# Kernel optimization log

Hardware: AMD Instinct MI355X
Metric: run time of the kernel (lower is better)

The kernel has to match this reference:

```python
import jax, jax.numpy as jnp
import numpy as np

TS = 6      # texture cube size (hard-coded in module)
S = 256     # image size (NMR default / ref image size)
DIST = 2.732


def _look_at(verts, eye):
    # NMR look_at: camera at eye, looking at origin, up=(0,1,0)
    eye = jnp.asarray(eye, verts.dtype)
    z = -eye / jnp.linalg.norm(eye)
    up = jnp.array([0.0, 1.0, 0.0], verts.dtype)
    x = jnp.cross(up, z)
    x = x / jnp.linalg.norm(x)
    y = jnp.cross(z, x)
    R = jnp.stack([x, y, z])          # rows = camera axes
    return (verts - eye) @ R.T


def _render(verts, faces, tex_flat, eye):
    # verts [V,3], faces [F,3] int, tex_flat [F*TS^3, 3] (tanh already applied)
    v = _look_at(verts, eye)
    fv = v[faces]                      # [F,3,3]
    p0, p1, p2 = fv[:, 0], fv[:, 1], fv[:, 2]
    ps = (2.0 * jnp.arange(S, dtype=verts.dtype) + 1.0 - S) / S
    PX = jnp.broadcast_to(ps[None, :], (S, S)).reshape(-1)      # x right
    PY = jnp.broadcast_to(-ps[:, None], (S, S)).reshape(-1)     # y up (row 0 = top)

    def edge(a, b):
        # signed edge function, [F,HW]
        return ((PX[None, :] - a[:, 0:1]) * (b[:, 1:2] - a[:, 1:2])
                - (PY[None, :] - a[:, 1:2]) * (b[:, 0:1] - a[:, 0:1]))

    e0 = edge(p1, p2)
    e1 = edge(p2, p0)
    e2 = edge(p0, p1)
    # per-face signed area (double area) [F,1]
    area = ((p1[:, 0] - p0[:, 0]) * (p2[:, 1] - p0[:, 1])
            - (p1[:, 1] - p0[:, 1]) * (p2[:, 0] - p0[:, 0]))[:, None]
    ok = jnp.abs(area) > 1e-8
    inv = jnp.where(ok, 1.0 / jnp.where(ok, area, 1.0), 0.0)
    w0, w1, w2 = e0 * inv, e1 * inv, e2 * inv            # barycentric weights
    inside = (w0 >= 0) & (w1 >= 0) & (w2 >= 0) & ok       # both windings (fill_back)
    z = w0 * p0[:, 2:3] + w1 * p1[:, 2:3] + w2 * p2[:, 2:3]
    depth = jnp.where(inside & (z > 0), z, jnp.inf)       # z-buffer candidates
    best = jnp.argmin(depth, axis=0)                      # [HW] winning face
    hit = jnp.take_along_axis(depth, best[None, :], axis=0)[0] < jnp.inf
    wb = jnp.stack([jnp.take_along_axis(w, best[None, :], axis=0)[0]
                    for w in (w0, w1, w2)], axis=-1)       # [HW,3]
    ti = jnp.clip(jnp.round(wb * (TS - 1)), 0, TS - 1).astype(jnp.int32)
    flat = ((best * TS + ti[:, 0]) * TS + ti[:, 1]) * TS + ti[:, 2]
    colors = tex_flat[flat]                                # [HW,3] gather
    img = jnp.where(hit[:, None], colors, 0.0)
    return img.reshape(S, S, 3).transpose(2, 0, 1)[None]   # [1,3,S,S]


def setup_inputs() -> dict:
    key = jax.random.key(0)
    k1, k2, k3, k4, k5 = jax.random.split(key, 5)
    V, F = 252, 500
    return {
        "vertices": jax.random.normal(k1, (1, V, 3), jnp.float32),
        "faces": jax.random.randint(k2, (1, F, 3), 0, V, jnp.int64),
        "textures": jax.random.normal(k3, (1, F, TS, TS, TS, 3), jnp.float32),
        "image_ref": jax.random.uniform(k4, (1, 3, S, S), jnp.float32),
        "image_ref_2": jax.random.uniform(k5, (1, 3, S, S), jnp.float32),
    }


def reference(vertices, faces, textures, image_ref, image_ref_2):
    tex_flat = jnp.tanh(textures[0]).reshape(-1, 3)
    v, f = vertices[0], faces[0]
    # eye = get_points_from_angles(2.732, 180, 0) -> (0, 0, +d)
    img1 = _render(v, f, tex_flat, jnp.array([0.0, 0.0, DIST], jnp.float32))
    loss_one_side = jnp.sum((img1 - image_ref) ** 2)
    # eye = get_points_from_angles(2.732, 0, 0) -> (0, 0, -d)
    img2 = _render(v, f, tex_flat, jnp.array([0.0, 0.0, -DIST], jnp.float32))
    loss_symmetric = jnp.sum((img2 - image_ref_2) ** 2)
    return (loss_one_side + loss_symmetric) / 2
```

## Files before the change

kernel.cpp:

```cpp
#include <hip/hip_runtime.h>
#include <math.h>

#define IMG_S 256
#define NPIX (IMG_S * IMG_S)
#define NFACE 500
#define NCHUNK 8
#define FPC_MAX 63
#define PPT 8
#define TSZ 6
#define DIST 2.732f

struct FaceCoef {
    float A0, B0, C0, A1, B1, C1, A2, B2, C2, Az, Bz, Cz;
};

__device__ __forceinline__ void edge_coef(float ax, float ay, float bx, float by,
                                          float inv, float& A, float& B, float& C) {
    float dy = by - ay;
    float dx = bx - ax;
    A = dy * inv;
    B = -dx * inv;
    C = (ay * dx - ax * dy) * inv;
}

__device__ __forceinline__ FaceCoef compute_face(const float* __restrict__ verts,
                                                 const int* __restrict__ faces,
                                                 int f, int view) {
    int i0 = faces[f * 3 + 0];
    int i1 = faces[f * 3 + 1];
    int i2 = faces[f * 3 + 2];

    float v0x = verts[i0 * 3 + 0], v0y = verts[i0 * 3 + 1], v0z = verts[i0 * 3 + 2];
    float v1x = verts[i1 * 3 + 0], v1y = verts[i1 * 3 + 1], v1z = verts[i1 * 3 + 2];
    float v2x = verts[i2 * 3 + 0], v2y = verts[i2 * 3 + 1], v2z = verts[i2 * 3 + 2];

    float p0x, p0y, p0z, p1x, p1y, p1z, p2x, p2y, p2z;
    if (view == 0) {
        p0x = -v0x; p0y = v0y; p0z = DIST - v0z;
        p1x = -v1x; p1y = v1y; p1z = DIST - v1z;
        p2x = -v2x; p2y = v2y; p2z = DIST - v2z;
    } else {
        p0x = v0x; p0y = v0y; p0z = v0z + DIST;
        p1x = v1x; p1y = v1y; p1z = v1z + DIST;
        p2x = v2x; p2y = v2y; p2z = v2z + DIST;
    }

    float area = (p1x - p0x) * (p2y - p0y) - (p1y - p0y) * (p2x - p0x);
    bool ok = fabsf(area) > 1e-8f;

    FaceCoef fc;
    if (ok) {
        float inv = 1.0f / area;
        edge_coef(p1x, p1y, p2x, p2y, inv, fc.A0, fc.B0, fc.C0);
        edge_coef(p2x, p2y, p0x, p0y, inv, fc.A1, fc.B1, fc.C1);
        edge_coef(p0x, p0y, p1x, p1y, inv, fc.A2, fc.B2, fc.C2);
        fc.Az = fc.A0 * p0z + fc.A1 * p1z + fc.A2 * p2z;
        fc.Bz = fc.B0 * p0z + fc.B1 * p1z + fc.B2 * p2z;
        fc.Cz = fc.C0 * p0z + fc.C1 * p1z + fc.C2 * p2z;
    } else {
        fc.A0 = fc.B0 = fc.A1 = fc.B1 = fc.A2 = fc.B2 = 0.0f;
        fc.C0 = fc.C1 = fc.C2 = -1.0f;
        fc.Az = fc.Bz = fc.Cz = 0.0f;
    }
    return fc;
}

__device__ __forceinline__ float pix_x(int ix) {
    return (2.0f * (float)ix + 1.0f - (float)IMG_S) * (1.0f / (float)IMG_S);
}
__device__ __forceinline__ float pix_y(int iy) {
    return -((2.0f * (float)iy + 1.0f - (float)IMG_S) * (1.0f / (float)IMG_S));
}

__global__ __launch_bounds__(256) void raster_chunk_kernel(
    const float* __restrict__ verts,
    const int*   __restrict__ faces,
    unsigned long long* __restrict__ packed_out)
{
    __shared__ float4 fc[FPC_MAX][3];
    const int tile  = blockIdx.x;
    const int chunk = blockIdx.y;
    const int view  = blockIdx.z;
    const int fbase = chunk * FPC_MAX;
    const int flen  = min(FPC_MAX, NFACE - fbase);

    if ((int)threadIdx.x < flen) {
        FaceCoef c = compute_face(verts, faces, fbase + (int)threadIdx.x, view);
        fc[threadIdx.x][0] = make_float4(c.A0, c.B0, c.C0, c.A1);
        fc[threadIdx.x][1] = make_float4(c.B1, c.C1, c.A2, c.B2);
        fc[threadIdx.x][2] = make_float4(c.C2, c.Az, c.Bz, c.Cz);
    }
    __syncthreads();

    const int ix = threadIdx.x;
    const float px = pix_x(ix);
    float py[PPT];
    #pragma unroll
    for (int k = 0; k < PPT; ++k) py[k] = pix_y(tile * PPT + k);

    float bestz[PPT];
    int   besti[PPT];
    #pragma unroll
    for (int k = 0; k < PPT; ++k) { bestz[k] = INFINITY; besti[k] = -1; }

    for (int f = 0; f < flen; ++f) {
        float4 q0 = fc[f][0];
        float4 q1 = fc[f][1];
        float4 q2 = fc[f][2];
        float d0 = fmaf(px, q0.x, q0.z);
        float d1 = fmaf(px, q0.w, q1.y);
        float d2 = fmaf(px, q1.z, q2.x);
        float dz = fmaf(px, q2.y, q2.w);
        #pragma unroll
        for (int k = 0; k < PPT; ++k) {
            float w0 = fmaf(q0.y, py[k], d0);
            float w1 = fmaf(q1.x, py[k], d1);
            float w2 = fmaf(q1.w, py[k], d2);
            float z  = fmaf(q2.z, py[k], dz);
            float wmin = fminf(w0, fminf(w1, w2));
            float s = fminf(z, bestz[k] - z);
            bool c = (wmin >= 0.0f) && (s > 0.0f);
            bestz[k] = c ? z : bestz[k];
            besti[k] = c ? f : besti[k];
        }
    }

    unsigned long long* __restrict__ outp =
        packed_out + (size_t)(view * NCHUNK + chunk) * NPIX + tile * (PPT * IMG_S) + ix;
    #pragma unroll
    for (int k = 0; k < PPT; ++k) {
        unsigned long long packed;
        if (besti[k] >= 0)
            packed = ((unsigned long long)__float_as_uint(bestz[k]) << 32) |
                     (unsigned int)(fbase + besti[k]);
        else
            packed = ~0ull;
        outp[k * IMG_S] = packed;
    }
}

__global__ __launch_bounds__(256) void shade_loss_kernel(
    const float* __restrict__ verts,
    const int*   __restrict__ faces,
    const float* __restrict__ tex,
    const float* __restrict__ ref0,
    const float* __restrict__ ref1,
    const unsigned long long* __restrict__ packed_in,
    float* __restrict__ partials)
{
    __shared__ float red[4];
    const int gid  = blockIdx.x * blockDim.x + threadIdx.x;
    const int view = gid >> 16;
    const int pix  = gid & (NPIX - 1);

    const unsigned long long* p = packed_in + (size_t)view * NCHUNK * NPIX + pix;
    unsigned long long best = p[0];
    #pragma unroll
    for (int c = 1; c < NCHUNK; ++c) {
        unsigned long long v = p[(size_t)c * NPIX];
        best = (v < best) ? v : best;
    }

    float c0 = 0.0f, c1 = 0.0f, c2 = 0.0f;
    if (best != ~0ull) {
        int fidx = (int)(best & 0xFFFFFFFFu);
        FaceCoef fcw = compute_face(verts, faces, fidx, view);
        const float px = pix_x(pix & (IMG_S - 1));
        const float py = pix_y(pix >> 8);
        float w0 = fmaf(px, fcw.A0, fmaf(py, fcw.B0, fcw.C0));
        float w1 = fmaf(px, fcw.A1, fmaf(py, fcw.B1, fcw.C1));
        float w2 = fmaf(px, fcw.A2, fmaf(py, fcw.B2, fcw.C2));
        int t0 = (int)fminf(fmaxf(rintf(w0 * (float)(TSZ - 1)), 0.0f), (float)(TSZ - 1));
        int t1 = (int)fminf(fmaxf(rintf(w1 * (float)(TSZ - 1)), 0.0f), (float)(TSZ - 1));
        int t2 = (int)fminf(fmaxf(rintf(w2 * (float)(TSZ - 1)), 0.0f), (float)(TSZ - 1));
        int flat = ((fidx * TSZ + t0) * TSZ + t1) * TSZ + t2;
        const float* t = tex + (long)flat * 3;
        c0 = tanhf(t[0]);
        c1 = tanhf(t[1]);
        c2 = tanhf(t[2]);
    }

    const float* __restrict__ ref = (view == 0) ? ref0 : ref1;
    float d0 = c0 - ref[0 * NPIX + pix];
    float d1 = c1 - ref[1 * NPIX + pix];
    float d2 = c2 - ref[2 * NPIX + pix];
    float acc = fmaf(d0, d0, fmaf(d1, d1, d2 * d2));

    for (int off = 32; off > 0; off >>= 1)
        acc += __shfl_down(acc, off, 64);
    int lane = threadIdx.x & 63;
    int wid = threadIdx.x >> 6;
    if (lane == 0) red[wid] = acc;
    __syncthreads();
    if (threadIdx.x == 0)
        partials[blockIdx.x] = red[0] + red[1] + red[2] + red[3];
}

__global__ __launch_bounds__(256) void reduce_kernel(const float* __restrict__ partials,
                                                     int n, float* __restrict__ out) {
    __shared__ float red[4];
    float v = 0.0f;
    for (int i = threadIdx.x; i < n; i += 256) v += partials[i];
    for (int off = 32; off > 0; off >>= 1)
        v += __shfl_down(v, off, 64);
    int lane = threadIdx.x & 63;
    int wid = threadIdx.x >> 6;
    if (lane == 0) red[wid] = v;
    __syncthreads();
    if (threadIdx.x == 0)
        out[0] = 0.5f * (red[0] + red[1] + red[2] + red[3]);
}

extern "C" void kernel_launch(void* const* d_in, const int* in_sizes, int n_in,
                              void* d_out, int out_size, void* d_ws, size_t ws_size,
                              hipStream_t stream) {
    const float* verts = (const float*)d_in[0];
    const int*   faces = (const int*)d_in[1];
    const float* tex   = (const float*)d_in[2];
    const float* ref0  = (const float*)d_in[3];
    const float* ref1  = (const float*)d_in[4];
    float* out = (float*)d_out;

    unsigned long long* packed = (unsigned long long*)d_ws;
    float* partials = (float*)((char*)d_ws + (size_t)2 * NCHUNK * NPIX * 8);

    dim3 grid1(NPIX / (256 * PPT), NCHUNK, 2);
    raster_chunk_kernel<<<grid1, 256, 0, stream>>>(verts, faces, packed);

    const int shade_blocks = (2 * NPIX) / 256;
    shade_loss_kernel<<<shade_blocks, 256, 0, stream>>>(verts, faces, tex, ref0, ref1,
                                                        packed, partials);
    reduce_kernel<<<1, 256, 0, stream>>>(partials, shade_blocks, out);
}
```

Before: 88.06 us.

## Precompute face coefficients in setup kernel, read uniformly, fuse final reduction via atomics

Adds a setup kernel that computes per-face edge and depth coefficients once per view into a padded global table. The raster kernel then reads them directly instead of recomputing them per block into shared memory, which removes that prologue and its barrier. The shade kernel reads the same table rather than rebuilding coefficients from vertices. The separate reduce kernel is replaced by per-block atomicAdd into an output zeroed by the setup kernel, which changes the floating-point summation order and makes it nondeterministic.

```diff
diff --git a/kernel.cpp b/kernel.cpp
--- a/kernel.cpp
+++ b/kernel.cpp
@@ -4,11 +4,14 @@
 #define IMG_S 256
 #define NPIX (IMG_S * IMG_S)
 #define NFACE 500
+#define NFACEPAD 512
 #define NCHUNK 8
-#define FPC_MAX 63
+#define FPC 64
 #define PPT 8
 #define TSZ 6
 #define DIST 2.732f
+#define CSTRIDE 16
+
 
 struct FaceCoef {
     float A0, B0, C0, A1, B1, C1, A2, B2, C2, Az, Bz, Cz;
@@ -72,25 +75,43 @@
     return -((2.0f * (float)iy + 1.0f - (float)IMG_S) * (1.0f / (float)IMG_S));
 }
 
-__global__ __launch_bounds__(256) void raster_chunk_kernel(
+__global__ __launch_bounds__(256) void setup_kernel(
     const float* __restrict__ verts,
     const int*   __restrict__ faces,
+    float* __restrict__ coef,
+    float* __restrict__ out)
+{
+    int gid = blockIdx.x * blockDim.x + threadIdx.x;
+    if (gid == 0) out[0] = 0.0f;
+    int view = gid >> 9;
+    int f    = gid & (NFACEPAD - 1);
+
+    FaceCoef c;
+    if (f < NFACE) {
+        c = compute_face(verts, faces, f, view);
+    } else {
+        c.A0 = c.B0 = c.A1 = c.B1 = c.A2 = c.B2 = 0.0f;
+        c.C0 = c.C1 = c.C2 = -1.0f;
+        c.Az = c.Bz = c.Cz = 0.0f;
+    }
+    float* p = coef + (size_t)(view * NFACEPAD + f) * CSTRIDE;
+    p[0] = c.A0; p[1] = c.B0; p[2] = c.C0;
+    p[3] = c.A1; p[4] = c.B1; p[5] = c.C1;
+    p[6] = c.A2; p[7] = c.B2; p[8] = c.C2;
+    p[9] = c.Az; p[10] = c.Bz; p[11] = c.Cz;
+    p[12] = 0.0f; p[13] = 0.0f; p[14] = 0.0f; p[15] = 0.0f;
+}
+
+__global__ __launch_bounds__(256) void raster_chunk_kernel(
+    const float* __restrict__ coef,
     unsigned long long* __restrict__ packed_out)
 {
-    __shared__ float4 fc[FPC_MAX][3];
     const int tile  = blockIdx.x;
     const int chunk = blockIdx.y;
     const int view  = blockIdx.z;
-    const int fbase = chunk * FPC_MAX;
-    const int flen  = min(FPC_MAX, NFACE - fbase);
-
-    if ((int)threadIdx.x < flen) {
-        FaceCoef c = compute_face(verts, faces, fbase + (int)threadIdx.x, view);
-        fc[threadIdx.x][0] = make_float4(c.A0, c.B0, c.C0, c.A1);
-        fc[threadIdx.x][1] = make_float4(c.B1, c.C1, c.A2, c.B2);
-        fc[threadIdx.x][2] = make_float4(c.C2, c.Az, c.Bz, c.Cz);
-    }
-    __syncthreads();
+    const int fbase = chunk * FPC;
+
+    const float* __restrict__ cf = coef + (size_t)(view * NFACEPAD + fbase) * CSTRIDE;
 
     const int ix = threadIdx.x;
     const float px = pix_x(ix);
@@ -103,25 +124,25 @@
     #pragma unroll
     for (int k = 0; k < PPT; ++k) { bestz[k] = INFINITY; besti[k] = -1; }
 
-    for (int f = 0; f < flen; ++f) {
-        float4 q0 = fc[f][0];
-        float4 q1 = fc[f][1];
-        float4 q2 = fc[f][2];
-        float d0 = fmaf(px, q0.x, q0.z);
-        float d1 = fmaf(px, q0.w, q1.y);
-        float d2 = fmaf(px, q1.z, q2.x);
-        float dz = fmaf(px, q2.y, q2.w);
+    #pragma unroll 2
+    for (int f = 0; f < FPC; ++f) {
+        const float* c = cf + f * CSTRIDE;
+        float B0 = c[1], B1 = c[4], B2 = c[7], Bz = c[10];
+        float d0 = fmaf(px, c[0], c[2]);
+        float d1 = fmaf(px, c[3], c[5]);
+        float d2 = fmaf(px, c[6], c[8]);
+        float dz = fmaf(px, c[9], c[11]);
         #pragma unroll
         for (int k = 0; k < PPT; ++k) {
-            float w0 = fmaf(q0.y, py[k], d0);
-            float w1 = fmaf(q1.x, py[k], d1);
-            float w2 = fmaf(q1.w, py[k], d2);
-            float z  = fmaf(q2.z, py[k], dz);
+            float w0 = fmaf(B0, py[k], d0);
+            float w1 = fmaf(B1, py[k], d1);
+            float w2 = fmaf(B2, py[k], d2);
+            float z  = fmaf(Bz, py[k], dz);
             float wmin = fminf(w0, fminf(w1, w2));
             float s = fminf(z, bestz[k] - z);
-            bool c = (wmin >= 0.0f) && (s > 0.0f);
-            bestz[k] = c ? z : bestz[k];
-            besti[k] = c ? f : besti[k];
+            bool cc = (wmin >= 0.0f) && (s > 0.0f);
+            bestz[k] = cc ? z : bestz[k];
+            besti[k] = cc ? f : besti[k];
         }
     }
 
@@ -140,13 +161,12 @@
 }
 
 __global__ __launch_bounds__(256) void shade_loss_kernel(
-    const float* __restrict__ verts,
-    const int*   __restrict__ faces,
+    const float* __restrict__ coef,
     const float* __restrict__ tex,
     const float* __restrict__ ref0,
     const float* __restrict__ ref1,
     const unsigned long long* __restrict__ packed_in,
-    float* __restrict__ partials)
+    float* __restrict__ out)
 {
     __shared__ float red[4];
     const int gid  = blockIdx.x * blockDim.x + threadIdx.x;
@@ -164,12 +184,12 @@
     float c0 = 0.0f, c1 = 0.0f, c2 = 0.0f;
     if (best != ~0ull) {
         int fidx = (int)(best & 0xFFFFFFFFu);
-        FaceCoef fcw = compute_face(verts, faces, fidx, view);
+        const float* c = coef + (size_t)(view * NFACEPAD + fidx) * CSTRIDE;
         const float px = pix_x(pix & (IMG_S - 1));
         const float py = pix_y(pix >> 8);
-        float w0 = fmaf(px, fcw.A0, fmaf(py, fcw.B0, fcw.C0));
-        float w1 = fmaf(px, fcw.A1, fmaf(py, fcw.B1, fcw.C1));
-        float w2 = fmaf(px, fcw.A2, fmaf(py, fcw.B2, fcw.C2));
+        float w0 = fmaf(c[1], py, fmaf(px, c[0], c[2]));
+        float w1 = fmaf(c[4], py, fmaf(px, c[3], c[5]));
+        float w2 = fmaf(c[7], py, fmaf(px, c[6], c[8]));
         int t0 = (int)fminf(fmaxf(rintf(w0 * (float)(TSZ - 1)), 0.0f), (float)(TSZ - 1));
         int t1 = (int)fminf(fmaxf(rintf(w1 * (float)(TSZ - 1)), 0.0f), (float)(TSZ - 1));
         int t2 = (int)fminf(fmaxf(rintf(w2 * (float)(TSZ - 1)), 0.0f), (float)(TSZ - 1));
@@ -193,22 +213,7 @@
     if (lane == 0) red[wid] = acc;
     __syncthreads();
     if (threadIdx.x == 0)
-        partials[blockIdx.x] = red[0] + red[1] + red[2] + red[3];
-}
-
-__global__ __launch_bounds__(256) void reduce_kernel(const float* __restrict__ partials,
-                                                     int n, float* __restrict__ out) {
-    __shared__ float red[4];
-    float v = 0.0f;
-    for (int i = threadIdx.x; i < n; i += 256) v += partials[i];
-    for (int off = 32; off > 0; off >>= 1)
-        v += __shfl_down(v, off, 64);
-    int lane = threadIdx.x & 63;
-    int wid = threadIdx.x >> 6;
-    if (lane == 0) red[wid] = v;
-    __syncthreads();
-    if (threadIdx.x == 0)
-        out[0] = 0.5f * (red[0] + red[1] + red[2] + red[3]);
+        atomicAdd(out, 0.5f * (red[0] + red[1] + red[2] + red[3]));
 }
 
 extern "C" void kernel_launch(void* const* d_in, const int* in_sizes, int n_in,
@@ -221,14 +226,16 @@
     const float* ref1  = (const float*)d_in[4];
     float* out = (float*)d_out;
 
-    unsigned long long* packed = (unsigned long long*)d_ws;
-    float* partials = (float*)((char*)d_ws + (size_t)2 * NCHUNK * NPIX * 8);
+    float* coef = (float*)d_ws;
+    unsigned long long* packed =
+        (unsigned long long*)((char*)d_ws + (size_t)2 * NFACEPAD * CSTRIDE * 4);
+
+    setup_kernel<<<4, 256, 0, stream>>>(verts, faces, coef, out);
 
     dim3 grid1(NPIX / (256 * PPT), NCHUNK, 2);
-    raster_chunk_kernel<<<grid1, 256, 0, stream>>>(verts, faces, packed);
+    raster_chunk_kernel<<<grid1, 256, 0, stream>>>(coef, packed);
 
     const int shade_blocks = (2 * NPIX) / 256;
-    shade_loss_kernel<<<shade_blocks, 256, 0, stream>>>(verts, faces, tex, ref0, ref1,
-                                                        packed, partials);
-    reduce_kernel<<<1, 256, 0, stream>>>(partials, shade_blocks, out);
-}
+    shade_loss_kernel<<<shade_blocks, 256, 0, stream>>>(coef, tex, ref0, ref1,
+                                                        packed, out);
+}
```

After: 109.9 us. 1.25x slower.

## Split faces into 16 padded chunks of 32 with prefetched coefficient loop

Applied to the files above, without the earlier changes.

Changes the face partitioning from 8 chunks of 63 to 16 chunks of 32 faces, doubling the raster grid so more blocks run in parallel. Faces past the end are padded with degenerate coefficients, so the loop has a fixed trip count and can be unrolled with a software-prefetch of the next face's shared-memory coefficients. The cost is that the shade kernel now reads and min-reduces twice as many packed candidates per pixel, and the workspace buffer doubles. The shade kernel's FMA order is also changed to match the raster evaluation order, so the recomputed barycentrics agree with those used for depth testing.

```diff
diff --git a/kernel.cpp b/kernel.cpp
--- a/kernel.cpp
+++ b/kernel.cpp
@@ -4,8 +4,8 @@
 #define IMG_S 256
 #define NPIX (IMG_S * IMG_S)
 #define NFACE 500
-#define NCHUNK 8
-#define FPC_MAX 63
+#define NCHUNK 16
+#define FPC 32
 #define PPT 8
 #define TSZ 6
 #define DIST 2.732f
@@ -77,15 +77,22 @@
     const int*   __restrict__ faces,
     unsigned long long* __restrict__ packed_out)
 {
-    __shared__ float4 fc[FPC_MAX][3];
+    __shared__ float4 fc[FPC][3];
     const int tile  = blockIdx.x;
     const int chunk = blockIdx.y;
     const int view  = blockIdx.z;
-    const int fbase = chunk * FPC_MAX;
-    const int flen  = min(FPC_MAX, NFACE - fbase);
-
-    if ((int)threadIdx.x < flen) {
-        FaceCoef c = compute_face(verts, faces, fbase + (int)threadIdx.x, view);
+    const int fbase = chunk * FPC;
+
+    if ((int)threadIdx.x < FPC) {
+        int f = fbase + (int)threadIdx.x;
+        FaceCoef c;
+        if (f < NFACE) {
+            c = compute_face(verts, faces, f, view);
+        } else {
+            c.A0 = c.B0 = c.A1 = c.B1 = c.A2 = c.B2 = 0.0f;
+            c.C0 = c.C1 = c.C2 = -1.0f;
+            c.Az = c.Bz = c.Cz = 0.0f;
+        }
         fc[threadIdx.x][0] = make_float4(c.A0, c.B0, c.C0, c.A1);
         fc[threadIdx.x][1] = make_float4(c.B1, c.C1, c.A2, c.B2);
         fc[threadIdx.x][2] = make_float4(c.C2, c.Az, c.Bz, c.Cz);
@@ -103,10 +110,13 @@
     #pragma unroll
     for (int k = 0; k < PPT; ++k) { bestz[k] = INFINITY; besti[k] = -1; }
 
-    for (int f = 0; f < flen; ++f) {
-        float4 q0 = fc[f][0];
-        float4 q1 = fc[f][1];
-        float4 q2 = fc[f][2];
+    float4 n0 = fc[0][0], n1 = fc[0][1], n2 = fc[0][2];
+    #pragma unroll 4
+    for (int f = 0; f < FPC; ++f) {
+        float4 q0 = n0, q1 = n1, q2 = n2;
+        int fn = (f + 1) & (FPC - 1);
+        n0 = fc[fn][0]; n1 = fc[fn][1]; n2 = fc[fn][2];
+
         float d0 = fmaf(px, q0.x, q0.z);
         float d1 = fmaf(px, q0.w, q1.y);
         float d2 = fmaf(px, q1.z, q2.x);
@@ -119,9 +129,9 @@
             float z  = fmaf(q2.z, py[k], dz);
             float wmin = fminf(w0, fminf(w1, w2));
             float s = fminf(z, bestz[k] - z);
-            bool c = (wmin >= 0.0f) && (s > 0.0f);
-            bestz[k] = c ? z : bestz[k];
-            besti[k] = c ? f : besti[k];
+            bool cc = (wmin >= 0.0f) && (s > 0.0f);
+            bestz[k] = cc ? z : bestz[k];
+            besti[k] = cc ? f : besti[k];
         }
     }
 
@@ -167,9 +177,9 @@
         FaceCoef fcw = compute_face(verts, faces, fidx, view);
         const float px = pix_x(pix & (IMG_S - 1));
         const float py = pix_y(pix >> 8);
-        float w0 = fmaf(px, fcw.A0, fmaf(py, fcw.B0, fcw.C0));
-        float w1 = fmaf(px, fcw.A1, fmaf(py, fcw.B1, fcw.C1));
-        float w2 = fmaf(px, fcw.A2, fmaf(py, fcw.B2, fcw.C2));
+        float w0 = fmaf(fcw.B0, py, fmaf(px, fcw.A0, fcw.C0));
+        float w1 = fmaf(fcw.B1, py, fmaf(px, fcw.A1, fcw.C1));
+        float w2 = fmaf(fcw.B2, py, fmaf(px, fcw.A2, fcw.C2));
         int t0 = (int)fminf(fmaxf(rintf(w0 * (float)(TSZ - 1)), 0.0f), (float)(TSZ - 1));
         int t1 = (int)fminf(fmaxf(rintf(w1 * (float)(TSZ - 1)), 0.0f), (float)(TSZ - 1));
         int t2 = (int)fminf(fmaxf(rintf(w2 * (float)(TSZ - 1)), 0.0f), (float)(TSZ - 1));
```

Measured after the change: 90.76 us. 3.1% more time.
